# Kernel optimization log

Measured on AMD Instinct MI355X. Metric: run time of the kernel, lower is better.

The kernel has to match this reference:

```python
import jax, jax.numpy as jnp
import numpy as np

V = 50257   # vocab_size
D = 128     # embed_dim
B = 1024    # batch of center words
C = 10      # context window size


def setup_inputs() -> dict:
    key = jax.random.key(0)
    ks = jax.random.split(key, 12)
    s = 0.05  # small init scale for linear weights
    return {
        "center_id": jax.random.randint(ks[0], (B,), 0, V),
        "context_ids": jax.random.randint(ks[1], (B, C), 0, V),
        "epsilon": jax.random.normal(ks[2], (D,), dtype=jnp.float32),
        # embedding tables init uniform(-1, 1) as in the torch module
        "emb": jax.random.uniform(ks[3], (V, D), minval=-1.0, maxval=1.0, dtype=jnp.float32),
        "prior_means": jax.random.uniform(ks[4], (V, D), minval=-1.0, maxval=1.0, dtype=jnp.float32),
        "prior_vars": jax.random.uniform(ks[5], (V, D), minval=-1.0, maxval=1.0, dtype=jnp.float32),
        "W_enc": jax.random.normal(ks[6], (2 * D, 2 * D), dtype=jnp.float32) * s,
        "b_enc": jnp.zeros((2 * D,), dtype=jnp.float32),
        "W_mean": jax.random.normal(ks[7], (2 * D, D), dtype=jnp.float32) * s,
        "b_mean": jnp.zeros((D,), dtype=jnp.float32),
        "W_var": jax.random.normal(ks[8], (2 * D, D), dtype=jnp.float32) * s,
        "b_var": jnp.zeros((D,), dtype=jnp.float32),
        "W_vocab": jax.random.normal(ks[9], (D, V), dtype=jnp.float32) * s,
        "b_vocab": jnp.zeros((V,), dtype=jnp.float32),
    }


def reference(center_id, context_ids, epsilon, emb, prior_means, prior_vars,
              W_enc, b_enc, W_mean, b_mean, W_var, b_var, W_vocab, b_vocab):
    ce = emb[center_id]                       # [B, D]
    cx = emb[context_ids]                     # [B, C, D]
    enc_in = jnp.concatenate(
        [jnp.broadcast_to(ce[:, None, :], cx.shape), cx], axis=-1)  # [B, C, 2D]
    h = jax.nn.relu(enc_in @ W_enc + b_enc).sum(axis=1)  # [B, 2D]
    mean = h @ W_mean + b_mean                           # [B, D]
    var = jax.nn.softplus(h @ W_var + b_var)             # [B, D] (diag cov s0)
    z = mean + jnp.exp(var / 2.0) * epsilon              # single shared epsilon [D]
    logits = z @ W_vocab + b_vocab                        # [B, V]
    logp = jax.nn.log_softmax(logits, axis=1)             # log(categorical)

    pm = prior_means[center_id]                           # m1 [B, D]
    pv = jax.nn.softplus(prior_vars[center_id])           # diag cov s1 [B, D]
    diff = pm - mean
    # closed-form diagonal Gaussian KL, identical math to the
    # trace/inverse/det formulation over diagflat matrices in the source
    kl = 0.5 * jnp.sum(var / pv + diff * diff / pv - 1.0
                       + jnp.log(pv) - jnp.log(var), axis=1)  # [B]

    # reconstruction: sum_k log categorical[i, context_ids[i, k]]
    rec = jnp.take_along_axis(logp, context_ids, axis=1).sum(axis=1)  # [B]

    return jnp.mean(rec - kl)
```

## Files before the change

### kernel.cpp

```cpp
#include <hip/hip_runtime.h>
#include <math.h>

#define VV 50257
#define VPAD 50304
#define DD 128
#define BB 1024
#define CC 10

typedef short bf16x8 __attribute__((ext_vector_type(8)));
typedef float f32x4 __attribute__((ext_vector_type(4)));

__device__ inline float bf2f(unsigned short u) {
    return __uint_as_float(((unsigned)u) << 16);
}
__device__ inline unsigned short f2bf(float f) {
    unsigned u = __float_as_uint(f);
    unsigned r = ((u >> 16) & 1) + 0x7FFF;
    return (unsigned short)((u + r) >> 16);
}


__global__ __launch_bounds__(256) void k_prep(
    const float* __restrict__ Wv, const float* __restrict__ W_enc,
    const float* __restrict__ W_mean, const float* __restrict__ W_var,
    unsigned short* __restrict__ WvP, unsigned short* __restrict__ WeP,
    unsigned short* __restrict__ Wmv)
{
    const int bid = blockIdx.x, tid = threadIdx.x;

    if (bid < 786) {
        __shared__ float tile[128][65];
        const int v0 = bid * 64;
#pragma unroll
        for (int i = 0; i < 32; ++i) {
            int idx = tid + i * 256;
            int k = idx >> 6, j = idx & 63;
            int v = v0 + j;
            tile[k][j] = (v < VV) ? Wv[(size_t)k * VV + v] : 0.f;
        }
        __syncthreads();
#pragma unroll
        for (int i = 0; i < 4; ++i) {
            int c = i * 256 + tid;
            int l15 = c & 15, q = (c >> 4) & 3, kI = (c >> 6) & 3, g = c >> 8;
            bf16x8 o;
#pragma unroll
            for (int e = 0; e < 8; ++e)
                o[e] = (short)f2bf(tile[kI * 32 + q * 8 + e][g * 16 + l15]);
            size_t vg = (size_t)bid * 4 + g;
            *(bf16x8*)(WvP + ((vg * 4 + kI) * 64 + q * 16 + l15) * 8) = o;
        }
        return;
    }

    if (bid < 802) {
        __shared__ float tl[256][17];
        const int jg = bid - 786;
#pragma unroll
        for (int i = 0; i < 16; ++i) {
            int idx = i * 256 + tid;
            int k = idx >> 4, j = idx & 15;
            tl[k][j] = W_enc[(size_t)k * 256 + jg * 16 + j];
        }
        __syncthreads();
#pragma unroll
        for (int i = 0; i < 2; ++i) {
            int c = i * 256 + tid;
            int l15 = c & 15, q = (c >> 4) & 3, kI = c >> 6;
            bf16x8 o;
#pragma unroll
            for (int e = 0; e < 8; ++e)
                o[e] = (short)f2bf(tl[kI * 32 + q * 8 + e][l15]);
            *(bf16x8*)(WeP + (((size_t)jg * 8 + kI) * 64 + q * 16 + l15) * 8) = o;
        }
        return;
    }

    const int b4 = bid - 802;
#pragma unroll
    for (int i = 0; i < 32; ++i) {
        int idx = b4 * 8192 + i * 256 + tid;
        unsigned short m = f2bf(W_mean[idx]);
        unsigned short v = f2bf(W_var[idx]);
        *(ushort2*)(Wmv + (size_t)idx * 2) = make_ushort2(m, v);
    }
}

#define AS_STRIDE 520
__global__ __launch_bounds__(256) void k_enc(
    const int* __restrict__ center_id, const int* __restrict__ context_ids,
    const float* __restrict__ emb, const unsigned short* __restrict__ WeP,
    const float* __restrict__ b_enc, unsigned short* __restrict__ enc_relu)
{
    __shared__ __align__(16) unsigned short As[32 * AS_STRIDE];
    __shared__ __align__(16) unsigned short Cs[64][136];
    const int tid  = threadIdx.x;
    const int lane = tid & 63;
    const int wid  = tid >> 6;
    const int wm   = wid & 1;
    const int wn   = wid >> 1;
    const int quad = lane >> 4;
    const int l15  = lane & 15;

    const int b0 = blockIdx.x * 64;
    const int c  = blockIdx.y;
    const int n0 = blockIdx.z * 128;

    const int rlane = tid >> 4;
    const int c8    = tid & 15;
    const int kIc   = c8 >> 2, qc = c8 & 3;
#pragma unroll
    for (int p = 0; p < 4; ++p) {
        int r = p * 16 + rlane;
        int rid_ce = center_id[b0 + r];
        int rid_cx = context_ids[(b0 + r) * CC + c];
        const float* s0 = emb + (size_t)rid_ce * 128 + c8 * 8;
        const float* s1 = emb + (size_t)rid_cx * 128 + c8 * 8;
        float4 a0 = *(const float4*)s0, a1 = *(const float4*)(s0 + 4);
        float4 b0v = *(const float4*)s1, b1v = *(const float4*)(s1 + 4);
        bf16x8 oa, ob;
        oa[0] = (short)f2bf(a0.x); oa[1] = (short)f2bf(a0.y);
        oa[2] = (short)f2bf(a0.z); oa[3] = (short)f2bf(a0.w);
        oa[4] = (short)f2bf(a1.x); oa[5] = (short)f2bf(a1.y);
        oa[6] = (short)f2bf(a1.z); oa[7] = (short)f2bf(a1.w);
        ob[0] = (short)f2bf(b0v.x); ob[1] = (short)f2bf(b0v.y);
        ob[2] = (short)f2bf(b0v.z); ob[3] = (short)f2bf(b0v.w);
        ob[4] = (short)f2bf(b1v.x); ob[5] = (short)f2bf(b1v.y);
        ob[6] = (short)f2bf(b1v.z); ob[7] = (short)f2bf(b1v.w);
        *(bf16x8*)(As + (size_t)(p * 8 + kIc) * AS_STRIDE + (qc * 16 + rlane) * 8) = oa;
        *(bf16x8*)(As + (size_t)(p * 8 + kIc + 4) * AS_STRIDE + (qc * 16 + rlane) * 8) = ob;
    }
    __syncthreads();

    float benc[4];
#pragma unroll
    for (int nt = 0; nt < 4; ++nt)
        benc[nt] = b_enc[n0 + wn * 64 + nt * 16 + l15];

    f32x4 acc[2][4];
#pragma unroll
    for (int mt = 0; mt < 2; ++mt)
#pragma unroll
        for (int nt = 0; nt < 4; ++nt) acc[mt][nt] = (f32x4){0.f, 0.f, 0.f, 0.f};

#pragma unroll
    for (int kI = 0; kI < 8; ++kI) {
        bf16x8 a[2], b[4];
#pragma unroll
        for (int mt = 0; mt < 2; ++mt)
            a[mt] = *(const bf16x8*)(As + (size_t)((wm * 2 + mt) * 8 + kI) * AS_STRIDE + lane * 8);
#pragma unroll
        for (int nt = 0; nt < 4; ++nt) {
            size_t jg = (size_t)blockIdx.z * 8 + wn * 4 + nt;
            b[nt] = *(const bf16x8*)(WeP + ((jg * 8 + kI) * 64 + lane) * 8);
        }
#pragma unroll
        for (int mt = 0; mt < 2; ++mt)
#pragma unroll
            for (int nt = 0; nt < 4; ++nt)
                acc[mt][nt] = __builtin_amdgcn_mfma_f32_16x16x32_bf16(
                    a[mt], b[nt], acc[mt][nt], 0, 0, 0);
    }

#pragma unroll
    for (int mt = 0; mt < 2; ++mt)
#pragma unroll
        for (int nt = 0; nt < 4; ++nt) {
            int col = wn * 64 + nt * 16 + l15;
#pragma unroll
            for (int reg = 0; reg < 4; ++reg) {
                int row = wm * 32 + mt * 16 + quad * 4 + reg;
                Cs[row][col] = f2bf(fmaxf(acc[mt][nt][reg] + benc[nt], 0.f));
            }
        }
    __syncthreads();
#pragma unroll
    for (int i = 0; i < 4; ++i) {
        int ch = i * 256 + tid;
        int row = ch >> 4, cc = ch & 15;
        bf16x8 v = *(const bf16x8*)&Cs[row][cc * 8];
        *(bf16x8*)(enc_relu + ((size_t)(b0 + row) * CC + c) * 256 + n0 + cc * 8) = v;
    }
}

__global__ __launch_bounds__(128) void k_latent(
    const unsigned short* __restrict__ enc_relu, const unsigned short* __restrict__ Wmv,
    const float* __restrict__ b_mean, const float* __restrict__ b_var,
    const float* __restrict__ epsilon,
    const int* __restrict__ center_id, const int* __restrict__ context_ids,
    const unsigned short* __restrict__ WvP, const float* __restrict__ bv,
    const float* __restrict__ prior_means, const float* __restrict__ prior_vars,
    unsigned short* __restrict__ z_pack, float* __restrict__ kl,
    float* __restrict__ ctxsum, float* __restrict__ out)
{
    __shared__ __align__(16) float hs[256];
    __shared__ float red[2];
    __shared__ float credp[CC][2];
    const int tid = threadIdx.x;
    const int b = blockIdx.x;
    const int wid = tid >> 6;

    if (b == 0 && tid == 0) out[0] = 0.f;

    {
        const int j = tid * 2;
        float s0 = 0.f, s1 = 0.f;
#pragma unroll
        for (int c = 0; c < CC; ++c) {
            ushort2 u = *(const ushort2*)(enc_relu + ((size_t)b * CC + c) * 256 + j);
            s0 += bf2f(u.x); s1 += bf2f(u.y);
        }
        hs[j] = s0; hs[j + 1] = s1;
    }
    __syncthreads();

    const int d = tid;
    float m  = b_mean[d];
    float vr = b_var[d];
    for (int k0 = 0; k0 < 256; k0 += 4) {
        float4 h4 = *(const float4*)&hs[k0];
#pragma unroll
        for (int kk = 0; kk < 4; ++kk) {
            float hk = ((const float*)&h4)[kk];
            ushort2 u = *(const ushort2*)(Wmv + ((size_t)(k0 + kk) * 128 + d) * 2);
            m  += hk * bf2f(u.x);
            vr += hk * bf2f(u.y);
        }
    }

    float var = (vr > 20.f) ? vr : log1pf(__expf(vr));
    float zd = m + __expf(0.5f * var) * epsilon[d];
    unsigned short zu = f2bf(zd);
    const int kIz = d >> 5, qz = (d >> 3) & 3, ez = d & 7;
    {
        const int bg = b >> 4, l15b = b & 15;
        z_pack[(((size_t)(bg * 4 + kIz)) * 64 + qz * 16 + l15b) * 8 + ez] = zu;
    }
    float zb = bf2f(zu);

    int cid = center_id[b];
    float pm  = prior_means[(size_t)cid * 128 + d];
    float pvr = prior_vars[(size_t)cid * 128 + d];
    float pv  = (pvr > 20.f) ? pvr : log1pf(__expf(pvr));
    float diff = pm - m;
    float t = var / pv + diff * diff / pv - 1.f + logf(pv) - logf(var);
#pragma unroll
    for (int off = 32; off; off >>= 1) t += __shfl_down(t, off, 64);
    if ((tid & 63) == 0) red[wid] = t;

    int cids[CC];
#pragma unroll
    for (int p = 0; p < CC; ++p) cids[p] = context_ids[b * CC + p];
    float cs[CC];
#pragma unroll
    for (int p = 0; p < CC; ++p) {
        int vg = cids[p] >> 4, l15v = cids[p] & 15;
        float w = bf2f(WvP[(((size_t)(vg * 4 + kIz)) * 64 + qz * 16 + l15v) * 8 + ez]);
        cs[p] = zb * w;
    }
#pragma unroll
    for (int p = 0; p < CC; ++p) {
#pragma unroll
        for (int off = 32; off; off >>= 1) cs[p] += __shfl_down(cs[p], off, 64);
    }
    if ((tid & 63) == 0) {
#pragma unroll
        for (int p = 0; p < CC; ++p) credp[p][wid] = cs[p];
    }
    __syncthreads();
    if (tid == 0) {
        kl[b] = 0.5f * (red[0] + red[1]);
        float c = 0.f;
#pragma unroll
        for (int p = 0; p < CC; ++p)
            c += credp[p][0] + credp[p][1] + bv[cids[p]];
        ctxsum[b] = c;
    }
}

__global__ __launch_bounds__(256) void k_lse(
    const unsigned short* __restrict__ z_pack, const unsigned short* __restrict__ WvP,
    const float* __restrict__ bv, float* __restrict__ partial)
{
    __shared__ float pl[2][128][20];
    const int tid  = threadIdx.x;
    const int lane = tid & 63;
    const int wid  = tid >> 6;
    const int wm   = wid & 1;
    const int wn   = wid >> 1;
    const int quad = lane >> 4;
    const int l15  = lane & 15;
    const int n0   = blockIdx.x * 128;
    const int mg   = blockIdx.y;

    bf16x8 bfr[4][4];
#pragma unroll
    for (int nt = 0; nt < 4; ++nt) {
        size_t vg = (size_t)blockIdx.x * 8 + wn * 4 + nt;
#pragma unroll
        for (int kI = 0; kI < 4; ++kI)
            bfr[nt][kI] = *(const bf16x8*)(WvP + ((vg * 4 + kI) * 64 + lane) * 8);
    }

    float bvf[4];
#pragma unroll
    for (int nt = 0; nt < 4; ++nt) {
        int n = n0 + wn * 64 + nt * 16 + l15;
        bvf[nt] = (n < VV) ? bv[n] : -__builtin_huge_valf();
    }

#pragma unroll
    for (int mi = 0; mi < 2; ++mi) {
        const int mi_g = mg * 2 + mi;

        f32x4 acc[4][4];
#pragma unroll
        for (int mt = 0; mt < 4; ++mt)
#pragma unroll
            for (int nt = 0; nt < 4; ++nt) acc[mt][nt] = (f32x4){0.f, 0.f, 0.f, 0.f};

#pragma unroll
        for (int kI = 0; kI < 4; ++kI) {
            bf16x8 afr[4];
#pragma unroll
            for (int mt = 0; mt < 4; ++mt) {
                size_t bg = (size_t)mi_g * 8 + wm * 4 + mt;
                afr[mt] = *(const bf16x8*)(z_pack + ((bg * 4 + kI) * 64 + lane) * 8);
            }
#pragma unroll
            for (int mt = 0; mt < 4; ++mt)
#pragma unroll
                for (int nt = 0; nt < 4; ++nt)
                    acc[mt][nt] = __builtin_amdgcn_mfma_f32_16x16x32_bf16(
                        afr[mt], bfr[nt][kI], acc[mt][nt], 0, 0, 0);
        }

#pragma unroll
        for (int mt = 0; mt < 4; ++mt)
#pragma unroll
            for (int reg = 0; reg < 4; ++reg) {
                float s = 0.f;
#pragma unroll
                for (int nt = 0; nt < 4; ++nt)
                    s += __expf(acc[mt][nt][reg] + bvf[nt]);
                pl[wn][wm * 64 + mt * 16 + quad * 4 + reg][l15] = s;
            }
        __syncthreads();
        if (tid < 128) {
            const float* p0 = &pl[0][tid][0];
            const float* p1 = &pl[1][tid][0];
            float4 a0 = *(const float4*)(p0);
            float4 a1 = *(const float4*)(p0 + 4);
            float4 a2 = *(const float4*)(p0 + 8);
            float4 a3 = *(const float4*)(p0 + 12);
            float4 b0 = *(const float4*)(p1);
            float4 b1 = *(const float4*)(p1 + 4);
            float4 b2 = *(const float4*)(p1 + 8);
            float4 b3 = *(const float4*)(p1 + 12);
            float tot = (a0.x + a0.y + a0.z + a0.w) + (a1.x + a1.y + a1.z + a1.w)
                      + (a2.x + a2.y + a2.z + a2.w) + (a3.x + a3.y + a3.z + a3.w)
                      + (b0.x + b0.y + b0.z + b0.w) + (b1.x + b1.y + b1.z + b1.w)
                      + (b2.x + b2.y + b2.z + b2.w) + (b3.x + b3.y + b3.z + b3.w);
            partial[(size_t)blockIdx.x * 1024 + mi_g * 128 + tid] = tot;
        }
        __syncthreads();
    }
}

__global__ __launch_bounds__(256) void k_reduce(
    const float* __restrict__ partial, const float* __restrict__ ctxsum,
    const float* __restrict__ kl, float* __restrict__ out)
{
    __shared__ float bred[4];
    const int tid = threadIdx.x;
    const int row = blockIdx.x * 16 + (tid >> 4);
    const int part = tid & 15;

    float s = 0.f;
    for (int vb = part; vb < 393; vb += 16)
        s += partial[(size_t)vb * 1024 + row];
    s += __shfl_xor(s, 1, 64);
    s += __shfl_xor(s, 2, 64);
    s += __shfl_xor(s, 4, 64);
    s += __shfl_xor(s, 8, 64);

    float v = 0.f;
    if (part == 0)
        v = ctxsum[row] - 10.f * logf(s) - kl[row];
    v += __shfl_xor(v, 16, 64);
    v += __shfl_xor(v, 32, 64);
    if ((tid & 63) == 0) bred[tid >> 6] = v;
    __syncthreads();
    if (tid == 0)
        atomicAdd(out, (bred[0] + bred[1] + bred[2] + bred[3]) * (1.f / 1024.f));
}

extern "C" void kernel_launch(void* const* d_in, const int* in_sizes, int n_in,
                              void* d_out, int out_size, void* d_ws, size_t ws_size,
                              hipStream_t stream)
{
    const int*   center_id   = (const int*)d_in[0];
    const int*   context_ids = (const int*)d_in[1];
    const float* epsilon     = (const float*)d_in[2];
    const float* emb         = (const float*)d_in[3];
    const float* prior_means = (const float*)d_in[4];
    const float* prior_vars  = (const float*)d_in[5];
    const float* W_enc       = (const float*)d_in[6];
    const float* b_enc       = (const float*)d_in[7];
    const float* W_mean      = (const float*)d_in[8];
    const float* b_mean      = (const float*)d_in[9];
    const float* W_var       = (const float*)d_in[10];
    const float* b_var       = (const float*)d_in[11];
    const float* W_vocab     = (const float*)d_in[12];
    const float* b_vocab     = (const float*)d_in[13];

    float* out = (float*)d_out;
    char*  ws  = (char*)d_ws;

    size_t off = 0;
    unsigned short* WvP      = (unsigned short*)(ws + off); off += 12877824;
    unsigned short* WeP      = (unsigned short*)(ws + off); off += 131072;
    unsigned short* Wmv      = (unsigned short*)(ws + off); off += 131072;
    unsigned short* z_pack   = (unsigned short*)(ws + off); off += 262144;
    unsigned short* enc_relu = (unsigned short*)(ws + off); off += 5242880;
    float*          kl       = (float*)(ws + off);          off += 4096;
    float*          ctxsum   = (float*)(ws + off);          off += 4096;
    float*          partial  = (float*)(ws + off);          off += 1609728;

    k_prep<<<806, 256, 0, stream>>>(W_vocab, W_enc, W_mean, W_var, WvP, WeP, Wmv);
    k_enc<<<dim3(16, 10, 2), 256, 0, stream>>>(center_id, context_ids, emb, WeP,
                                               b_enc, enc_relu);
    k_latent<<<1024, 128, 0, stream>>>(enc_relu, Wmv, b_mean, b_var, epsilon,
                                       center_id, context_ids, WvP, b_vocab,
                                       prior_means, prior_vars, z_pack, kl,
                                       ctxsum, out);
    k_lse<<<dim3(393, 4), 256, 0, stream>>>(z_pack, WvP, b_vocab, partial);
    k_reduce<<<64, 256, 0, stream>>>(partial, ctxsum, kl, out);
}
```

Measured before the change: 208.6 us.

## Overlap W_vocab repacking with encoder GEMM and split latent K-loop

Moves the large W_vocab bf16 repack out of the prep kernel and into the same launch as the encoder GEMM, so both run concurrently on spare CUs. The prep kernel keeps only the small W_enc and W_mean/W_var conversions. k_latent now uses 256 threads and splits the mean/var dot-product K dimension across two halves, combining them through shared memory. k_lse is relaunched on a 3D grid with early-exit padding, which changes the block scheduling order. The costs are extra shared-memory traffic, a larger merged shared-memory footprint, and half the k_latent threads sitting idle during the epilogue.

```diff
diff --git a/kernel.cpp b/kernel.cpp
--- a/kernel.cpp
+++ b/kernel.cpp
@@ -20,17 +20,60 @@
 }
 
 
-__global__ __launch_bounds__(256) void k_prep(
-    const float* __restrict__ Wv, const float* __restrict__ W_enc,
-    const float* __restrict__ W_mean, const float* __restrict__ W_var,
-    unsigned short* __restrict__ WvP, unsigned short* __restrict__ WeP,
+__global__ __launch_bounds__(256) void k_prep0(
+    const float* __restrict__ W_enc, const float* __restrict__ W_mean,
+    const float* __restrict__ W_var, unsigned short* __restrict__ WeP,
     unsigned short* __restrict__ Wmv)
 {
+    __shared__ float tl[256][17];
     const int bid = blockIdx.x, tid = threadIdx.x;
 
-    if (bid < 786) {
-        __shared__ float tile[128][65];
-        const int v0 = bid * 64;
+    if (bid < 16) {
+        const int jg = bid;
+#pragma unroll
+        for (int i = 0; i < 16; ++i) {
+            int idx = i * 256 + tid;
+            int k = idx >> 4, j = idx & 15;
+            tl[k][j] = W_enc[(size_t)k * 256 + jg * 16 + j];
+        }
+        __syncthreads();
+#pragma unroll
+        for (int i = 0; i < 2; ++i) {
+            int c = i * 256 + tid;
+            int l15 = c & 15, q = (c >> 4) & 3, kI = c >> 6;
+            bf16x8 o;
+#pragma unroll
+            for (int e = 0; e < 8; ++e)
+                o[e] = (short)f2bf(tl[kI * 32 + q * 8 + e][l15]);
+            *(bf16x8*)(WeP + (((size_t)jg * 8 + kI) * 64 + q * 16 + l15) * 8) = o;
+        }
+        return;
+    }
+
+    const int b4 = bid - 16;
+#pragma unroll
+    for (int i = 0; i < 32; ++i) {
+        int idx = b4 * 8192 + i * 256 + tid;
+        unsigned short m = f2bf(W_mean[idx]);
+        unsigned short v = f2bf(W_var[idx]);
+        *(ushort2*)(Wmv + (size_t)idx * 2) = make_ushort2(m, v);
+    }
+}
+
+#define AS_STRIDE 520
+__global__ __launch_bounds__(256) void k_main(
+    const int* __restrict__ center_id, const int* __restrict__ context_ids,
+    const float* __restrict__ emb, const unsigned short* __restrict__ WeP,
+    const float* __restrict__ b_enc, const float* __restrict__ Wv,
+    unsigned short* __restrict__ WvP, unsigned short* __restrict__ enc_relu)
+{
+    __shared__ __align__(16) unsigned char smraw[50688];
+    const int bid = blockIdx.x, tid = threadIdx.x;
+
+    if (bid >= 320) {
+        float (*tile)[65] = (float (*)[65])smraw;
+        const int s = bid - 320;
+        const int v0 = s * 64;
 #pragma unroll
         for (int i = 0; i < 32; ++i) {
             int idx = tid + i * 256;
@@ -47,54 +90,15 @@
 #pragma unroll
             for (int e = 0; e < 8; ++e)
                 o[e] = (short)f2bf(tile[kI * 32 + q * 8 + e][g * 16 + l15]);
-            size_t vg = (size_t)bid * 4 + g;
+            size_t vg = (size_t)s * 4 + g;
             *(bf16x8*)(WvP + ((vg * 4 + kI) * 64 + q * 16 + l15) * 8) = o;
         }
         return;
     }
 
-    if (bid < 802) {
-        __shared__ float tl[256][17];
-        const int jg = bid - 786;
-#pragma unroll
-        for (int i = 0; i < 16; ++i) {
-            int idx = i * 256 + tid;
-            int k = idx >> 4, j = idx & 15;
-            tl[k][j] = W_enc[(size_t)k * 256 + jg * 16 + j];
-        }
-        __syncthreads();
-#pragma unroll
-        for (int i = 0; i < 2; ++i) {
-            int c = i * 256 + tid;
-            int l15 = c & 15, q = (c >> 4) & 3, kI = c >> 6;
-            bf16x8 o;
-#pragma unroll
-            for (int e = 0; e < 8; ++e)
-                o[e] = (short)f2bf(tl[kI * 32 + q * 8 + e][l15]);
-            *(bf16x8*)(WeP + (((size_t)jg * 8 + kI) * 64 + q * 16 + l15) * 8) = o;
-        }
-        return;
-    }
-
-    const int b4 = bid - 802;
-#pragma unroll
-    for (int i = 0; i < 32; ++i) {
-        int idx = b4 * 8192 + i * 256 + tid;
-        unsigned short m = f2bf(W_mean[idx]);
-        unsigned short v = f2bf(W_var[idx]);
-        *(ushort2*)(Wmv + (size_t)idx * 2) = make_ushort2(m, v);
-    }
-}
-
-#define AS_STRIDE 520
-__global__ __launch_bounds__(256) void k_enc(
-    const int* __restrict__ center_id, const int* __restrict__ context_ids,
-    const float* __restrict__ emb, const unsigned short* __restrict__ WeP,
-    const float* __restrict__ b_enc, unsigned short* __restrict__ enc_relu)
-{
-    __shared__ __align__(16) unsigned short As[32 * AS_STRIDE];
-    __shared__ __align__(16) unsigned short Cs[64][136];
-    const int tid  = threadIdx.x;
+    unsigned short* As = (unsigned short*)smraw;
+    unsigned short (*Cs)[136] = (unsigned short (*)[136])(smraw + 33280);
+
     const int lane = tid & 63;
     const int wid  = tid >> 6;
     const int wm   = wid & 1;
@@ -102,9 +106,11 @@
     const int quad = lane >> 4;
     const int l15  = lane & 15;
 
-    const int b0 = blockIdx.x * 64;
-    const int c  = blockIdx.y;
-    const int n0 = blockIdx.z * 128;
+    const int bt = bid & 15;
+    const int c  = (bid >> 4) % 10;
+    const int zt = bid / 160;
+    const int b0 = bt * 64;
+    const int n0 = zt * 128;
 
     const int rlane = tid >> 4;
     const int c8    = tid & 15;
@@ -151,7 +157,7 @@
             a[mt] = *(const bf16x8*)(As + (size_t)((wm * 2 + mt) * 8 + kI) * AS_STRIDE + lane * 8);
 #pragma unroll
         for (int nt = 0; nt < 4; ++nt) {
-            size_t jg = (size_t)blockIdx.z * 8 + wn * 4 + nt;
+            size_t jg = (size_t)zt * 8 + wn * 4 + nt;
             b[nt] = *(const bf16x8*)(WeP + ((jg * 8 + kI) * 64 + lane) * 8);
         }
 #pragma unroll
@@ -183,7 +189,7 @@
     }
 }
 
-__global__ __launch_bounds__(128) void k_latent(
+__global__ __launch_bounds__(256) void k_latent(
     const unsigned short* __restrict__ enc_relu, const unsigned short* __restrict__ Wmv,
     const float* __restrict__ b_mean, const float* __restrict__ b_var,
     const float* __restrict__ epsilon,
@@ -194,86 +200,96 @@
     float* __restrict__ ctxsum, float* __restrict__ out)
 {
     __shared__ __align__(16) float hs[256];
+    __shared__ float mpart[128], vpart[128];
     __shared__ float red[2];
     __shared__ float credp[CC][2];
     const int tid = threadIdx.x;
     const int b = blockIdx.x;
-    const int wid = tid >> 6;
 
     if (b == 0 && tid == 0) out[0] = 0.f;
 
     {
-        const int j = tid * 2;
-        float s0 = 0.f, s1 = 0.f;
-#pragma unroll
-        for (int c = 0; c < CC; ++c) {
-            ushort2 u = *(const ushort2*)(enc_relu + ((size_t)b * CC + c) * 256 + j);
-            s0 += bf2f(u.x); s1 += bf2f(u.y);
-        }
-        hs[j] = s0; hs[j + 1] = s1;
-    }
-    __syncthreads();
-
-    const int d = tid;
-    float m  = b_mean[d];
-    float vr = b_var[d];
-    for (int k0 = 0; k0 < 256; k0 += 4) {
-        float4 h4 = *(const float4*)&hs[k0];
+        float s0 = 0.f;
+#pragma unroll
+        for (int c = 0; c < CC; ++c)
+            s0 += bf2f(enc_relu[((size_t)b * CC + c) * 256 + tid]);
+        hs[tid] = s0;
+    }
+    __syncthreads();
+
+    const int d = tid & 127;
+    const int half = tid >> 7;
+    float m  = half ? 0.f : b_mean[d];
+    float vr = half ? 0.f : b_var[d];
+    const int kbase = half << 7;
+    for (int k0 = 0; k0 < 128; k0 += 4) {
+        float4 h4 = *(const float4*)&hs[kbase + k0];
 #pragma unroll
         for (int kk = 0; kk < 4; ++kk) {
             float hk = ((const float*)&h4)[kk];
-            ushort2 u = *(const ushort2*)(Wmv + ((size_t)(k0 + kk) * 128 + d) * 2);
+            ushort2 u = *(const ushort2*)(Wmv + ((size_t)(kbase + k0 + kk) * 128 + d) * 2);
             m  += hk * bf2f(u.x);
             vr += hk * bf2f(u.y);
         }
     }
-
-    float var = (vr > 20.f) ? vr : log1pf(__expf(vr));
-    float zd = m + __expf(0.5f * var) * epsilon[d];
-    unsigned short zu = f2bf(zd);
-    const int kIz = d >> 5, qz = (d >> 3) & 3, ez = d & 7;
-    {
-        const int bg = b >> 4, l15b = b & 15;
-        z_pack[(((size_t)(bg * 4 + kIz)) * 64 + qz * 16 + l15b) * 8 + ez] = zu;
-    }
-    float zb = bf2f(zu);
-
-    int cid = center_id[b];
-    float pm  = prior_means[(size_t)cid * 128 + d];
-    float pvr = prior_vars[(size_t)cid * 128 + d];
-    float pv  = (pvr > 20.f) ? pvr : log1pf(__expf(pvr));
-    float diff = pm - m;
-    float t = var / pv + diff * diff / pv - 1.f + logf(pv) - logf(var);
-#pragma unroll
-    for (int off = 32; off; off >>= 1) t += __shfl_down(t, off, 64);
-    if ((tid & 63) == 0) red[wid] = t;
-
-    int cids[CC];
-#pragma unroll
-    for (int p = 0; p < CC; ++p) cids[p] = context_ids[b * CC + p];
-    float cs[CC];
-#pragma unroll
-    for (int p = 0; p < CC; ++p) {
-        int vg = cids[p] >> 4, l15v = cids[p] & 15;
-        float w = bf2f(WvP[(((size_t)(vg * 4 + kIz)) * 64 + qz * 16 + l15v) * 8 + ez]);
-        cs[p] = zb * w;
-    }
-#pragma unroll
-    for (int p = 0; p < CC; ++p) {
-#pragma unroll
-        for (int off = 32; off; off >>= 1) cs[p] += __shfl_down(cs[p], off, 64);
-    }
-    if ((tid & 63) == 0) {
-#pragma unroll
-        for (int p = 0; p < CC; ++p) credp[p][wid] = cs[p];
+    if (half) { mpart[d] = m; vpart[d] = vr; }
+    __syncthreads();
+
+    if (!half) {
+        const int wid = tid >> 6;
+        m  += mpart[d];
+        vr += vpart[d];
+
+        float var = (vr > 20.f) ? vr : log1pf(__expf(vr));
+        float zd = m + __expf(0.5f * var) * epsilon[d];
+        unsigned short zu = f2bf(zd);
+        const int kIz = d >> 5, qz = (d >> 3) & 3, ez = d & 7;
+        {
+            const int bg = b >> 4, l15b = b & 15;
+            z_pack[(((size_t)(bg * 4 + kIz)) * 64 + qz * 16 + l15b) * 8 + ez] = zu;
+        }
+        float zb = bf2f(zu);
+
+        int cid = center_id[b];
+        float pm  = prior_means[(size_t)cid * 128 + d];
+        float pvr = prior_vars[(size_t)cid * 128 + d];
+        float pv  = (pvr > 20.f) ? pvr : log1pf(__expf(pvr));
+        float diff = pm - m;
+        float t = var / pv + diff * diff / pv - 1.f + logf(pv) - logf(var);
+#pragma unroll
+        for (int off = 32; off; off >>= 1) t += __shfl_down(t, off, 64);
+        if ((tid & 63) == 0) red[wid] = t;
+
+        int cids[CC];
+#pragma unroll
+        for (int p = 0; p < CC; ++p) cids[p] = context_ids[b * CC + p];
+        float cs[CC];
+#pragma unroll
+        for (int p = 0; p < CC; ++p) {
+            int vg = cids[p] >> 4, l15v = cids[p] & 15;
+            float w = bf2f(WvP[(((size_t)(vg * 4 + kIz)) * 64 + qz * 16 + l15v) * 8 + ez]);
+            cs[p] = zb * w;
+        }
+#pragma unroll
+        for (int p = 0; p < CC; ++p) {
+#pragma unroll
+            for (int off = 32; off; off >>= 1) cs[p] += __shfl_down(cs[p], off, 64);
+        }
+        if ((tid & 63) == 0) {
+#pragma unroll
+            for (int p = 0; p < CC; ++p) credp[p][wid] = cs[p];
+        }
     }
     __syncthreads();
     if (tid == 0) {
         kl[b] = 0.5f * (red[0] + red[1]);
         float c = 0.f;
-#pragma unroll
-        for (int p = 0; p < CC; ++p)
-            c += credp[p][0] + credp[p][1] + bv[cids[p]];
+        int cid0;
+#pragma unroll
+        for (int p = 0; p < CC; ++p) {
+            cid0 = context_ids[b * CC + p];
+            c += credp[p][0] + credp[p][1] + bv[cid0];
+        }
         ctxsum[b] = c;
     }
 }
@@ -283,6 +299,10 @@
     const float* __restrict__ bv, float* __restrict__ partial)
 {
     __shared__ float pl[2][128][20];
+    const int x = blockIdx.x + 8 * blockIdx.y;
+    if (x >= 393) return;
+    const int mg = blockIdx.z;
+
     const int tid  = threadIdx.x;
     const int lane = tid & 63;
     const int wid  = tid >> 6;
@@ -290,13 +310,12 @@
     const int wn   = wid >> 1;
     const int quad = lane >> 4;
     const int l15  = lane & 15;
-    const int n0   = blockIdx.x * 128;
-    const int mg   = blockIdx.y;
+    const int n0   = x * 128;
 
     bf16x8 bfr[4][4];
 #pragma unroll
     for (int nt = 0; nt < 4; ++nt) {
-        size_t vg = (size_t)blockIdx.x * 8 + wn * 4 + nt;
+        size_t vg = (size_t)x * 8 + wn * 4 + nt;
 #pragma unroll
         for (int kI = 0; kI < 4; ++kI)
             bfr[nt][kI] = *(const bf16x8*)(WvP + ((vg * 4 + kI) * 64 + lane) * 8);
@@ -361,7 +380,7 @@
                       + (a2.x + a2.y + a2.z + a2.w) + (a3.x + a3.y + a3.z + a3.w)
                       + (b0.x + b0.y + b0.z + b0.w) + (b1.x + b1.y + b1.z + b1.w)
                       + (b2.x + b2.y + b2.z + b2.w) + (b3.x + b3.y + b3.z + b3.w);
-            partial[(size_t)blockIdx.x * 1024 + mi_g * 128 + tid] = tot;
+            partial[(size_t)x * 1024 + mi_g * 128 + tid] = tot;
         }
         __syncthreads();
     }
@@ -427,13 +446,13 @@
     float*          ctxsum   = (float*)(ws + off);          off += 4096;
     float*          partial  = (float*)(ws + off);          off += 1609728;
 
-    k_prep<<<806, 256, 0, stream>>>(W_vocab, W_enc, W_mean, W_var, WvP, WeP, Wmv);
-    k_enc<<<dim3(16, 10, 2), 256, 0, stream>>>(center_id, context_ids, emb, WeP,
-                                               b_enc, enc_relu);
-    k_latent<<<1024, 128, 0, stream>>>(enc_relu, Wmv, b_mean, b_var, epsilon,
+    k_prep0<<<20, 256, 0, stream>>>(W_enc, W_mean, W_var, WeP, Wmv);
+    k_main<<<1106, 256, 0, stream>>>(center_id, context_ids, emb, WeP, b_enc,
+                                     W_vocab, WvP, enc_relu);
+    k_latent<<<1024, 256, 0, stream>>>(enc_relu, Wmv, b_mean, b_var, epsilon,
                                        center_id, context_ids, WvP, b_vocab,
                                        prior_means, prior_vars, z_pack, kl,
                                        ctxsum, out);
-    k_lse<<<dim3(393, 4), 256, 0, stream>>>(z_pack, WvP, b_vocab, partial);
+    k_lse<<<dim3(8, 50, 4), 256, 0, stream>>>(z_pack, WvP, b_vocab, partial);
     k_reduce<<<64, 256, 0, stream>>>(partial, ctxsum, kl, out);
 }
```

Result: faster. 200.2 us (-4.0%).
